# Optimization experiments

Measured on AMD Instinct MI355X. Metric: run time of the kernel, lower is better.

Reference implementation:

```python
import jax, jax.numpy as jnp
import numpy as np

B, S, DIM, H = 2, 2048, 512, 8  # batch, seq_len, model dim, num_heads


def setup_inputs() -> dict:
    key = jax.random.key(0)
    ks = jax.random.split(key, 8)
    s = 0.02
    return {
        "queries": jax.random.normal(ks[0], (B, S, DIM), dtype=jnp.float32),
        "keys": jax.random.normal(ks[1], (B, S, DIM), dtype=jnp.float32),
        "Wq": jax.random.normal(ks[2], (DIM, DIM), dtype=jnp.float32) * s,
        "bq": jax.random.normal(ks[3], (DIM,), dtype=jnp.float32) * s,
        "Wk": jax.random.normal(ks[4], (DIM, DIM), dtype=jnp.float32) * s,
        "bk": jax.random.normal(ks[5], (DIM,), dtype=jnp.float32) * s,
        "Wv": jax.random.normal(ks[6], (DIM, DIM), dtype=jnp.float32) * s,
        "bv": jax.random.normal(ks[7], (DIM,), dtype=jnp.float32) * s,
        "causality": 1,
    }


def _split_heads(x):
    # torch: cat(chunk(x, H, dim=2), dim=0): [B,S,D] -> [H*B, S, d], head-major
    b, s, dmod = x.shape
    d = dmod // H
    return x.reshape(b, s, H, d).transpose(2, 0, 1, 3).reshape(H * b, s, d)


def reference(queries, keys, Wq, bq, Wk, bk, Wv, bv, causality):
    b, sq, dim = queries.shape
    sk = keys.shape[1]
    d = dim // H

    Q = queries @ Wq.T + bq
    K = keys @ Wk.T + bk
    V = keys @ Wv.T + bv
    Q_, K_, V_ = _split_heads(Q), _split_heads(K), _split_heads(V)  # [H*B, S, d]

    scores = jnp.einsum("nqd,nkd->nqk", Q_, K_) / jnp.sqrt(jnp.float32(d))

    # key padding mask from raw keys: sign(sum |keys|) -> [B,Sk] -> [H*B,1,Sk]
    key_masks = jnp.sign(jnp.sum(jnp.abs(keys), axis=-1))
    key_masks = jnp.tile(key_masks, (H, 1))[:, None, :]
    scores = jnp.where(key_masks == 0, -jnp.inf, scores)

    if causality:
        tril = jnp.tril(jnp.ones((sq, sk), dtype=bool))
        scores = jnp.where(tril[None, :, :], scores, -jnp.inf)

    attn = jax.nn.softmax(scores, axis=-1)
    attn = jnp.nan_to_num(attn, nan=0.0, posinf=0.0, neginf=0.0)

    # query padding mask: [B,Sq] -> [H*B,Sq,1], multiplicative
    query_masks = jnp.sign(jnp.sum(jnp.abs(queries), axis=-1))
    query_masks = jnp.tile(query_masks, (H, 1))[:, :, None]
    attn = attn * query_masks

    # attention_weights: stack H chunks along dim 1 -> [B, H, Sq, Sk]
    attention_weights = attn.reshape(H, b, sq, sk).transpose(1, 0, 2, 3)

    # dropout in eval mode = identity
    out = jnp.einsum("nqk,nkd->nqd", attn, V_)  # [H*B, Sq, d]
    # merge heads back: cat(chunk(out, H, dim=0), dim=2)
    out = out.reshape(H, b, sq, d).transpose(1, 2, 0, 3).reshape(b, sq, dim)
    return out, attention_weights
```

## Files before the change

kernel.cpp:

```cpp
#include <hip/hip_runtime.h>
#include <math.h>

#define B_ 2
#define S_ 2048
#define DIM_ 512
#define H_ 8
#define DH_ 64
#define QBLK 16
#define KTILE 32
#define PSTRIDE 2056

typedef __bf16 bf16x8 __attribute__((ext_vector_type(8)));
typedef float f32x4 __attribute__((ext_vector_type(4)));
typedef float vf4 __attribute__((ext_vector_type(4)));
typedef unsigned short ushort_t;
typedef ushort_t ushort8 __attribute__((ext_vector_type(8)));

__device__ __forceinline__ ushort_t f2bf(float f) {
    union { float f; unsigned u; } v; v.f = f;
    unsigned u = v.u;
    return (ushort_t)((u + 0x7FFFu + ((u >> 16) & 1u)) >> 16);
}
__device__ __forceinline__ float bf2f(ushort_t u) {
    union { unsigned u; float f; } v; v.u = ((unsigned)u) << 16;
    return v.f;
}

__global__ __launch_bounds__(256) void convert_kernel(
    const float* __restrict__ q, const float* __restrict__ k,
    const float* __restrict__ wq, const float* __restrict__ wk,
    const float* __restrict__ wv,
    ushort_t* qbf, ushort_t* kbf, ushort_t* wqb, ushort_t* wkb, ushort_t* wvb)
{
    const float* src; ushort_t* dst; int n;
    switch (blockIdx.y) {
        case 0: src = q;  dst = qbf; n = B_ * S_ * DIM_; break;
        case 1: src = k;  dst = kbf; n = B_ * S_ * DIM_; break;
        case 2: src = wq; dst = wqb; n = DIM_ * DIM_; break;
        case 3: src = wk; dst = wkb; n = DIM_ * DIM_; break;
        default: src = wv; dst = wvb; n = DIM_ * DIM_; break;
    }
    int i4 = blockIdx.x * 256 + threadIdx.x;
    if (i4 * 4 >= n) return;
    float4 v = ((const float4*)src)[i4];
    ushort4 o;
    o.x = f2bf(v.x); o.y = f2bf(v.y); o.z = f2bf(v.z); o.w = f2bf(v.w);
    ((ushort4*)dst)[i4] = o;
}

__global__ __launch_bounds__(256) void proj_mfma_kernel(
    const ushort_t* __restrict__ Qin, const ushort_t* __restrict__ Kin,
    const ushort_t* __restrict__ Wqb, const float* __restrict__ bq,
    const ushort_t* __restrict__ Wkb, const float* __restrict__ bk,
    const ushort_t* __restrict__ Wvb, const float* __restrict__ bv,
    ushort_t* __restrict__ Qh, ushort_t* __restrict__ Kh, ushort_t* __restrict__ Vt)
{
    __shared__ float T[64][68];

    const int which = blockIdx.z;
    const ushort_t* A = (which == 0) ? Qin : Kin;
    const ushort_t* W = (which == 0) ? Wqb : (which == 1 ? Wkb : Wvb);
    const float* bias = (which == 0) ? bq : (which == 1 ? bk : bv);

    const int r0 = blockIdx.x * 64;
    const int h  = blockIdx.y;
    const int c0 = h * DH_;
    const int tid = threadIdx.x;
    const int w = tid >> 6, l = tid & 63;
    const int lr = l & 15, lg = l >> 4;

    f32x4 acc[4] = {};
    const ushort_t* arow  = A + (size_t)(r0 + w * 16 + lr) * DIM_ + lg * 8;
    const ushort_t* wrow0 = W + (size_t)(c0 + lr) * DIM_ + lg * 8;

#pragma unroll 4
    for (int ks = 0; ks < DIM_ / 32; ++ks) {
        bf16x8 a = *(const bf16x8*)(arow + ks * 32);
#pragma unroll
        for (int ct = 0; ct < 4; ++ct) {
            bf16x8 bfr = *(const bf16x8*)(wrow0 + (size_t)ct * 16 * DIM_ + ks * 32);
            acc[ct] = __builtin_amdgcn_mfma_f32_16x16x32_bf16(a, bfr, acc[ct], 0, 0, 0);
        }
    }

    if (which < 2) {
        ushort_t* OUT = (which == 0) ? Qh : Kh;
#pragma unroll
        for (int ct = 0; ct < 4; ++ct) {
            int d = ct * 16 + lr;
            float bi = bias[c0 + d];
#pragma unroll
            for (int reg = 0; reg < 4; ++reg) {
                int rr = r0 + w * 16 + lg * 4 + reg;
                int bb = rr >> 11, s = rr & (S_ - 1);
                int n = h * B_ + bb;
                OUT[((size_t)n * S_ + s) * DH_ + d] = f2bf(acc[ct][reg] + bi);
            }
        }
    } else {
#pragma unroll
        for (int ct = 0; ct < 4; ++ct) {
            int d = ct * 16 + lr;
            float bi = bias[c0 + d];
#pragma unroll
            for (int reg = 0; reg < 4; ++reg)
                T[w * 16 + lg * 4 + reg][d] = acc[ct][reg] + bi;
        }
        __syncthreads();
        int d = tid & 63, sc = tid >> 6;
        int rr = r0 + sc * 16;
        int bb = rr >> 11, s = rr & (S_ - 1);
        int n = h * B_ + bb;
        ushort8 o[2];
#pragma unroll
        for (int i = 0; i < 16; ++i)
            ((ushort_t*)o)[i] = f2bf(T[sc * 16 + i][d]);
        ushort8* dst = (ushort8*)(Vt + ((size_t)n * DH_ + d) * S_ + s);
        dst[0] = o[0];
        dst[1] = o[1];
    }
}

__global__ __launch_bounds__(256, 2) void attn_mfma_kernel(
    const ushort_t* __restrict__ Qh, const ushort_t* __restrict__ Kh,
    const ushort_t* __restrict__ Vt, const int* __restrict__ causp,
    float* __restrict__ outp, float* __restrict__ attnw)
{
    __shared__ ushort_t Pl[QBLK][PSTRIDE];
    __shared__ float sums[4][QBLK];

    const int bid = blockIdx.x;
    const int swz = (bid & 7) * 256 + (bid >> 3);
    const int n = swz >> 7;
    const int qt = swz & 127;
    const int h = n / B_, b = n % B_;
    const int q0 = qt * QBLK;
    const int causal = causp[0];
    const int tid = threadIdx.x;
    const int w = tid >> 6, l = tid & 63;
    const int lr = l & 15, lg = l >> 4;

    const int kmax = causal ? (q0 + QBLK) : S_;
    const int kend = ((kmax + KTILE - 1) / KTILE) * KTILE;

    float* attrow = attnw + ((size_t)((b * H_ + h) * S_ + q0)) * S_;

    if (kend < S_) {
        int zc = (S_ - kend) >> 2;
        vf4 z = {0.f, 0.f, 0.f, 0.f};
        for (int idx = tid; idx < QBLK * zc; idx += 256) {
            int r = idx / zc, c4 = (idx % zc) << 2;
            __builtin_nontemporal_store(z, (vf4*)&attrow[(size_t)r * S_ + kend + c4]);
        }
    }

    const ushort_t* qrow = Qh + ((size_t)n * S_ + q0 + lr) * DH_ + lg * 8;
    bf16x8 qa0 = *(const bf16x8*)(qrow);
    bf16x8 qa1 = *(const bf16x8*)(qrow + 32);

    const ushort_t* Kbase = Kh + (size_t)n * S_ * DH_;

    float pl[4] = {0.f, 0.f, 0.f, 0.f};
    for (int kc = w * KTILE; kc < kend; kc += 4 * KTILE) {
        const ushort_t* kra = Kbase + (size_t)(kc + lr) * DH_ + lg * 8;
        const ushort_t* krb = kra + (size_t)16 * DH_;
        f32x4 accA = {}, accB = {};
        accA = __builtin_amdgcn_mfma_f32_16x16x32_bf16(qa0, *(const bf16x8*)(kra),      accA, 0, 0, 0);
        accA = __builtin_amdgcn_mfma_f32_16x16x32_bf16(qa1, *(const bf16x8*)(kra + 32), accA, 0, 0, 0);
        accB = __builtin_amdgcn_mfma_f32_16x16x32_bf16(qa0, *(const bf16x8*)(krb),      accB, 0, 0, 0);
        accB = __builtin_amdgcn_mfma_f32_16x16x32_bf16(qa1, *(const bf16x8*)(krb + 32), accB, 0, 0, 0);
#pragma unroll
        for (int reg = 0; reg < 4; ++reg) {
            int row = lg * 4 + reg;
            int qq = q0 + row;
            int kA = kc + lr, kB = kA + 16;
            float eA = (!causal || kA <= qq) ? __expf(accA[reg] * 0.125f) : 0.f;
            float eB = (!causal || kB <= qq) ? __expf(accB[reg] * 0.125f) : 0.f;
            pl[reg] += eA + eB;
            Pl[row][kA] = f2bf(eA);
            Pl[row][kB] = f2bf(eB);
        }
    }

#pragma unroll
    for (int reg = 0; reg < 4; ++reg) {
        float v = pl[reg];
        v += __shfl_xor(v, 1); v += __shfl_xor(v, 2);
        v += __shfl_xor(v, 4); v += __shfl_xor(v, 8);
        if (lr == 0) sums[w][lg * 4 + reg] = v;
    }
    __syncthreads();

    {
        int row = tid >> 4, cl = (tid & 15) << 2;
        float invw = 1.f / (sums[0][row] + sums[1][row] + sums[2][row] + sums[3][row]);
        float* ar = attrow + (size_t)row * S_;
        for (int c = cl; c < kend; c += 64) {
            ushort4 pv = *(const ushort4*)&Pl[row][c];
            vf4 o;
            o.x = bf2f(pv.x) * invw;
            o.y = bf2f(pv.y) * invw;
            o.z = bf2f(pv.z) * invw;
            o.w = bf2f(pv.w) * invw;
            __builtin_nontemporal_store(o, (vf4*)&ar[c]);
        }
    }

    float inv_r[4];
#pragma unroll
    for (int reg = 0; reg < 4; ++reg) {
        int row = lg * 4 + reg;
        inv_r[reg] = 1.f / (sums[0][row] + sums[1][row] + sums[2][row] + sums[3][row]);
    }
    f32x4 oacc = {};
    const ushort_t* Vbase = Vt + (size_t)n * DH_ * S_ + (size_t)(w * 16 + lr) * S_;
    for (int kt = 0; kt < kend; kt += KTILE) {
        bf16x8 pa = *(const bf16x8*)&Pl[lr][kt + lg * 8];
        bf16x8 vb = *(const bf16x8*)(Vbase + kt + lg * 8);
        oacc = __builtin_amdgcn_mfma_f32_16x16x32_bf16(pa, vb, oacc, 0, 0, 0);
    }
#pragma unroll
    for (int reg = 0; reg < 4; ++reg) {
        int qq = q0 + lg * 4 + reg;
        __builtin_nontemporal_store(oacc[reg] * inv_r[reg],
            &outp[((size_t)b * S_ + qq) * DIM_ + h * DH_ + w * 16 + lr]);
    }
}

extern "C" void kernel_launch(void* const* d_in, const int* in_sizes, int n_in,
                              void* d_out, int out_size, void* d_ws, size_t ws_size,
                              hipStream_t stream) {
    const float* queries = (const float*)d_in[0];
    const float* keys    = (const float*)d_in[1];
    const float* Wq = (const float*)d_in[2];
    const float* bq = (const float*)d_in[3];
    const float* Wk = (const float*)d_in[4];
    const float* bk = (const float*)d_in[5];
    const float* Wv = (const float*)d_in[6];
    const float* bv = (const float*)d_in[7];
    const int*   caus = (const int*)d_in[8];

    char* ws = (char*)d_ws;
    ushort_t* Qin_bf = (ushort_t*)ws;  ws += (size_t)B_*S_*DIM_*2;
    ushort_t* Kin_bf = (ushort_t*)ws;  ws += (size_t)B_*S_*DIM_*2;
    ushort_t* Wqb = (ushort_t*)ws;     ws += (size_t)DIM_*DIM_*2;
    ushort_t* Wkb = (ushort_t*)ws;     ws += (size_t)DIM_*DIM_*2;
    ushort_t* Wvb = (ushort_t*)ws;     ws += (size_t)DIM_*DIM_*2;
    ushort_t* Qh = (ushort_t*)ws;      ws += (size_t)H_*B_*S_*DH_*2;
    ushort_t* Kh = (ushort_t*)ws;      ws += (size_t)H_*B_*S_*DH_*2;
    ushort_t* Vt = (ushort_t*)ws;      ws += (size_t)H_*B_*DH_*S_*2;

    float* outp  = (float*)d_out;
    float* attnw = outp + (size_t)B_ * S_ * DIM_;

    convert_kernel<<<dim3(2048, 5), 256, 0, stream>>>(
        queries, keys, Wq, Wk, Wv, Qin_bf, Kin_bf, Wqb, Wkb, Wvb);

    proj_mfma_kernel<<<dim3(64, 8, 3), 256, 0, stream>>>(
        Qin_bf, Kin_bf, Wqb, bq, Wkb, bk, Wvb, bv, Qh, Kh, Vt);

    attn_mfma_kernel<<<2048, 256, 0, stream>>>(Qh, Kh, Vt, caus, outp, attnw);
}
```

Measured before the change: 158.1 us.

## Enlarge projection row tile, reverse causal tile order, widen attention-weight stores

The projection kernel now computes 128 rows per block with two A fragments reusing each weight fragment, halving the grid and weight reloads. The attention kernel reverses query-tile order so the heaviest causal tiles launch first, improving tail balance. Attention-weight writeback now has each wave handle whole rows with 8-element LDS reads and paired 16-byte stores, and bf16 conversion uses the native cast. The larger projection tile raises LDS and register use and reduces block count.

Measured after the change: 156.4 us. About the same (-1.1%).

```diff
diff --git a/kernel.cpp b/kernel.cpp
--- a/kernel.cpp
+++ b/kernel.cpp
@@ -55,69 +55,76 @@
     const ushort_t* __restrict__ Wvb, const float* __restrict__ bv,
     ushort_t* __restrict__ Qh, ushort_t* __restrict__ Kh, ushort_t* __restrict__ Vt)
 {
-    __shared__ float T[64][68];
+    __shared__ float T[128][68];
 
     const int which = blockIdx.z;
     const ushort_t* A = (which == 0) ? Qin : Kin;
     const ushort_t* W = (which == 0) ? Wqb : (which == 1 ? Wkb : Wvb);
     const float* bias = (which == 0) ? bq : (which == 1 ? bk : bv);
 
-    const int r0 = blockIdx.x * 64;
+    const int r0 = blockIdx.x * 128;
     const int h  = blockIdx.y;
     const int c0 = h * DH_;
     const int tid = threadIdx.x;
     const int w = tid >> 6, l = tid & 63;
     const int lr = l & 15, lg = l >> 4;
 
-    f32x4 acc[4] = {};
-    const ushort_t* arow  = A + (size_t)(r0 + w * 16 + lr) * DIM_ + lg * 8;
+    f32x4 acc[2][4] = {};
+    const ushort_t* arow0 = A + (size_t)(r0 + w * 32 + lr) * DIM_ + lg * 8;
+    const ushort_t* arow1 = arow0 + (size_t)16 * DIM_;
     const ushort_t* wrow0 = W + (size_t)(c0 + lr) * DIM_ + lg * 8;
 
 #pragma unroll 4
     for (int ks = 0; ks < DIM_ / 32; ++ks) {
-        bf16x8 a = *(const bf16x8*)(arow + ks * 32);
+        bf16x8 a0 = *(const bf16x8*)(arow0 + ks * 32);
+        bf16x8 a1 = *(const bf16x8*)(arow1 + ks * 32);
 #pragma unroll
         for (int ct = 0; ct < 4; ++ct) {
             bf16x8 bfr = *(const bf16x8*)(wrow0 + (size_t)ct * 16 * DIM_ + ks * 32);
-            acc[ct] = __builtin_amdgcn_mfma_f32_16x16x32_bf16(a, bfr, acc[ct], 0, 0, 0);
-        }
-    }
+            acc[0][ct] = __builtin_amdgcn_mfma_f32_16x16x32_bf16(a0, bfr, acc[0][ct], 0, 0, 0);
+            acc[1][ct] = __builtin_amdgcn_mfma_f32_16x16x32_bf16(a1, bfr, acc[1][ct], 0, 0, 0);
+        }
+    }
+
+    const int bb = r0 >> 11;
+    const int s0 = r0 & (S_ - 1);
+    const int n = h * B_ + bb;
 
     if (which < 2) {
         ushort_t* OUT = (which == 0) ? Qh : Kh;
 #pragma unroll
-        for (int ct = 0; ct < 4; ++ct) {
-            int d = ct * 16 + lr;
-            float bi = bias[c0 + d];
-#pragma unroll
-            for (int reg = 0; reg < 4; ++reg) {
-                int rr = r0 + w * 16 + lg * 4 + reg;
-                int bb = rr >> 11, s = rr & (S_ - 1);
-                int n = h * B_ + bb;
-                OUT[((size_t)n * S_ + s) * DH_ + d] = f2bf(acc[ct][reg] + bi);
+        for (int rg = 0; rg < 2; ++rg) {
+#pragma unroll
+            for (int ct = 0; ct < 4; ++ct) {
+                int d = ct * 16 + lr;
+                float bi = bias[c0 + d];
+#pragma unroll
+                for (int reg = 0; reg < 4; ++reg) {
+                    int s = s0 + w * 32 + rg * 16 + lg * 4 + reg;
+                    OUT[((size_t)n * S_ + s) * DH_ + d] = f2bf(acc[rg][ct][reg] + bi);
+                }
             }
         }
     } else {
 #pragma unroll
-        for (int ct = 0; ct < 4; ++ct) {
-            int d = ct * 16 + lr;
-            float bi = bias[c0 + d];
-#pragma unroll
-            for (int reg = 0; reg < 4; ++reg)
-                T[w * 16 + lg * 4 + reg][d] = acc[ct][reg] + bi;
+        for (int rg = 0; rg < 2; ++rg) {
+#pragma unroll
+            for (int ct = 0; ct < 4; ++ct) {
+                int d = ct * 16 + lr;
+                float bi = bias[c0 + d];
+#pragma unroll
+                for (int reg = 0; reg < 4; ++reg)
+                    T[w * 32 + rg * 16 + lg * 4 + reg][d] = acc[rg][ct][reg] + bi;
+            }
         }
         __syncthreads();
         int d = tid & 63, sc = tid >> 6;
-        int rr = r0 + sc * 16;
-        int bb = rr >> 11, s = rr & (S_ - 1);
-        int n = h * B_ + bb;
-        ushort8 o[2];
-#pragma unroll
-        for (int i = 0; i < 16; ++i)
-            ((ushort_t*)o)[i] = f2bf(T[sc * 16 + i][d]);
-        ushort8* dst = (ushort8*)(Vt + ((size_t)n * DH_ + d) * S_ + s);
-        dst[0] = o[0];
-        dst[1] = o[1];
+        ushort8 o[4];
+#pragma unroll
+        for (int i = 0; i < 32; ++i)
+            ((ushort_t*)o)[i] = f2bf(T[sc * 32 + i][d]);
+        ushort8* dst = (ushort8*)(Vt + ((size_t)n * DH_ + d) * S_ + s0 + sc * 32);
+        dst[0] = o[0]; dst[1] = o[1]; dst[2] = o[2]; dst[3] = o[3];
     }
 }
 
@@ -132,7 +139,7 @@
     const int bid = blockIdx.x;
     const int swz = (bid & 7) * 256 + (bid >> 3);
     const int n = swz >> 7;
-    const int qt = swz & 127;
+    const int qt = 127 - (swz & 127);
     const int h = n / B_, b = n % B_;
     const int q0 = qt * QBLK;
     const int causal = causp[0];
@@ -177,8 +184,9 @@
             float eA = (!causal || kA <= qq) ? __expf(accA[reg] * 0.125f) : 0.f;
             float eB = (!causal || kB <= qq) ? __expf(accB[reg] * 0.125f) : 0.f;
             pl[reg] += eA + eB;
-            Pl[row][kA] = f2bf(eA);
-            Pl[row][kB] = f2bf(eB);
+            __bf16 vA = (__bf16)eA, vB = (__bf16)eB;
+            Pl[row][kA] = *(ushort_t*)&vA;
+            Pl[row][kB] = *(ushort_t*)&vB;
         }
     }
 
@@ -191,18 +199,20 @@
     }
     __syncthreads();
 
-    {
-        int row = tid >> 4, cl = (tid & 15) << 2;
+#pragma unroll
+    for (int rr = 0; rr < 4; ++rr) {
+        int row = w * 4 + rr;
         float invw = 1.f / (sums[0][row] + sums[1][row] + sums[2][row] + sums[3][row]);
         float* ar = attrow + (size_t)row * S_;
-        for (int c = cl; c < kend; c += 64) {
-            ushort4 pv = *(const ushort4*)&Pl[row][c];
-            vf4 o;
-            o.x = bf2f(pv.x) * invw;
-            o.y = bf2f(pv.y) * invw;
-            o.z = bf2f(pv.z) * invw;
-            o.w = bf2f(pv.w) * invw;
-            __builtin_nontemporal_store(o, (vf4*)&ar[c]);
+        for (int c = l * 8; c < kend; c += 512) {
+            ushort8 pv = *(const ushort8*)&Pl[row][c];
+            vf4 o0, o1;
+            o0.x = bf2f(pv[0]) * invw; o0.y = bf2f(pv[1]) * invw;
+            o0.z = bf2f(pv[2]) * invw; o0.w = bf2f(pv[3]) * invw;
+            o1.x = bf2f(pv[4]) * invw; o1.y = bf2f(pv[5]) * invw;
+            o1.z = bf2f(pv[6]) * invw; o1.w = bf2f(pv[7]) * invw;
+            __builtin_nontemporal_store(o0, (vf4*)&ar[c]);
+            __builtin_nontemporal_store(o1, (vf4*)&ar[c + 4]);
         }
     }
 
@@ -256,7 +266,7 @@
     convert_kernel<<<dim3(2048, 5), 256, 0, stream>>>(
         queries, keys, Wq, Wk, Wv, Qin_bf, Kin_bf, Wqb, Wkb, Wvb);
 
-    proj_mfma_kernel<<<dim3(64, 8, 3), 256, 0, stream>>>(
+    proj_mfma_kernel<<<dim3(32, 8, 3), 256, 0, stream>>>(
         Qin_bf, Kin_bf, Wqb, bq, Wkb, bk, Wvb, bv, Qh, Kh, Vt);
 
     attn_mfma_kernel<<<2048, 256, 0, stream>>>(Qh, Kh, Vt, caus, outp, attnw);
```
